# Kernel tuning notes

Measured on AMD Instinct MI355X. Metric: run time of the kernel, lower is better.

The kernel has to match this reference:

```python
import jax, jax.numpy as jnp
import numpy as np

N_FR, N_FV, N_REL, N_VAL, N_KN = 512, 512, 256, 256, 512
TOPK_FR, TOPK_FV, TOPK_REL, TOPK_VAL = 8, 8, 4, 6
EPS = 1e-8


def setup_inputs() -> dict:
    key = jax.random.key(0)
    k1, k2, k3, k4 = jax.random.split(key, 4)
    B, S, D, DS = 8, 2048, 2048, 64
    N = N_FR + N_FV + N_REL + N_VAL + N_KN  # 2304
    return {
        "x": jax.random.normal(k1, (B, S, D), dtype=jnp.float32),
        "importance": jax.random.uniform(k2, (B, S), dtype=jnp.float32),
        "W": jax.random.normal(k3, (DS, D), dtype=jnp.float32) * (1.0 / np.sqrt(D)),
        "b": jnp.zeros((DS,), dtype=jnp.float32),
        "neuron_emb": jax.random.normal(k4, (N, DS), dtype=jnp.float32) * 0.02,
    }


def _topk_sparsify(w, k):
    # w: [B, n] -> keep top-k values, zero the rest, renormalize to sum 1
    vals, idx = jax.lax.top_k(w, k)
    B = w.shape[0]
    sparse = jnp.zeros_like(w).at[jnp.arange(B)[:, None], idx].set(vals)
    return sparse / (sparse.sum(axis=-1, keepdims=True) + EPS)


def reference(x, importance, W, b, neuron_emb):
    # Projection (nn.Linear): [B,S,d_space]; dropout is identity in eval mode
    h = jnp.einsum('bsd,kd->bsk', x, W) + b
    # Normalized neuron embeddings (F.normalize along dim=-1)
    emb = neuron_emb / jnp.linalg.norm(neuron_emb, axis=-1, keepdims=True)
    # All routing logits in one shot: [B, S, total_neurons]
    all_logits = jnp.einsum('bsk,nk->bsn', h, emb)

    fr_end = N_FR
    fv_end = N_FR + N_FV
    rel_end = fv_end + N_REL
    val_end = rel_end + N_VAL

    fr_pref = jax.nn.softmax(all_logits[..., :fr_end], axis=-1)
    fv_pref = jax.nn.softmax(all_logits[..., fr_end:fv_end], axis=-1)
    rel_pref = jax.nn.softmax(all_logits[..., fv_end:rel_end], axis=-1)  # shared by Q and K
    val_pref = jax.nn.softmax(all_logits[..., rel_end:val_end], axis=-1)

    def dense(pref):
        return jnp.einsum('bs,bsn->bn', importance, pref)

    fr_w = _topk_sparsify(dense(fr_pref), TOPK_FR)
    fv_w = _topk_sparsify(dense(fv_pref), TOPK_FV)
    rel_d = dense(rel_pref)
    rq_w = _topk_sparsify(rel_d, TOPK_REL)
    rk_w = rq_w  # relational_Q and relational_K slices are identical
    val_w = _topk_sparsify(dense(val_pref), TOPK_VAL)

    # Concatenate the five per-batch routing weight vectors: [B, 512+512+256+256+256]
    return jnp.concatenate([fr_w, fv_w, rq_w, rk_w, val_w], axis=-1)
```

## Files before the change

kernel.cpp:

```cpp
#include <hip/hip_runtime.h>
#include <hip/hip_bf16.h>
#include <hip/hip_fp16.h>

#define B_    8
#define S_    2048
#define D_    2048
#define DS_   64
#define NUSED 1536
#define TOK   16384

typedef __attribute__((ext_vector_type(8))) short bf16x8;
typedef __attribute__((ext_vector_type(4))) float f32x4;

static constexpr int WS_ETF   = 0;
static constexpr int WS_HT    = 98304;
static constexpr int WS_HF    = 2195456;
static constexpr int WS_PART  = 3244032;
static constexpr int WS_PART2 = 4816896;
static constexpr int WS_WF    = 4915200;

__device__ inline short bf_hi(float f, float& rhi) {
    __hip_bfloat16 h = __float2bfloat16(f);
    rhi = __bfloat162float(h);
    return __builtin_bit_cast(short, h);
}
__device__ inline short bf_of(float f) {
    __hip_bfloat16 h = __float2bfloat16(f);
    return __builtin_bit_cast(short, h);
}
__device__ inline int sliceOfTile(int tile) {
    return tile < 32 ? 0 : tile < 64 ? 1 : tile < 80 ? 2 : 3;
}

__launch_bounds__(256)
__global__ void k_wsplit(const float* __restrict__ W, short* __restrict__ wfrag) {
    const int t = threadIdx.x, kstep = blockIdx.x;
    const int msub = t >> 6, lane = t & 63;
    const int m = msub * 16 + (lane & 15);
    const float* wp = W + m * D_ + kstep * 32 + (lane >> 4) * 8;
    float4 a = *reinterpret_cast<const float4*>(wp);
    float4 b = *reinterpret_cast<const float4*>(wp + 4);
    float f[8] = {a.x, a.y, a.z, a.w, b.x, b.y, b.z, b.w};
    bf16x8 hi, lo;
#pragma unroll
    for (int j = 0; j < 8; ++j) {
        float r;
        hi[j] = bf_hi(f[j], r);
        lo[j] = bf_of(f[j] - r);
    }
    short* dst = wfrag + (((kstep << 2) | msub) * 64 + lane) * 16;
    *reinterpret_cast<bf16x8*>(dst)     = hi;
    *reinterpret_cast<bf16x8*>(dst + 8) = lo;
}

__launch_bounds__(128)
__global__ void k_embpack(const float* __restrict__ emb, short* __restrict__ etfrag) {
    __shared__ float red[16][8];
    __shared__ float rn[16];
    const int tid = threadIdx.x;
    const int kh = tid >> 6, lane = tid & 63;
    const int tile = blockIdx.x;
    const int nl = lane & 15;
    const int n = tile * 16 + nl;
    const int kb = kh * 32 + (lane >> 4) * 8;
    const float* ep = emb + n * DS_ + kb;
    float4 a = *reinterpret_cast<const float4*>(ep);
    float4 b = *reinterpret_cast<const float4*>(ep + 4);
    float f[8] = {a.x, a.y, a.z, a.w, b.x, b.y, b.z, b.w};
    float ss = 0.f;
#pragma unroll
    for (int j = 0; j < 8; ++j) ss += f[j] * f[j];
    red[nl][kh * 4 + (lane >> 4)] = ss;
    __syncthreads();
    if (tid < 16) {
        float s = 0.f;
#pragma unroll
        for (int j = 0; j < 8; ++j) s += red[tid][j];
        rn[tid] = 1.0f / sqrtf(s);
    }
    __syncthreads();
    const float r0 = rn[nl];
    bf16x8 hi, lo;
#pragma unroll
    for (int j = 0; j < 8; ++j) {
        float v = f[j] * r0, r;
        hi[j] = bf_hi(v, r);
        lo[j] = bf_of(v - r);
    }
    short* dst = etfrag + (size_t)((tile * 2 + kh) * 64 + lane) * 16;
    *reinterpret_cast<bf16x8*>(dst)     = hi;
    *reinterpret_cast<bf16x8*>(dst + 8) = lo;
}

#define MFMA16(A, Bv, C) __builtin_amdgcn_mfma_f32_16x16x32_bf16(A, Bv, C, 0, 0, 0)

__launch_bounds__(256, 2)
__global__ void k_gemm1(const float* __restrict__ x, const short* __restrict__ wfrag,
                        float* __restrict__ htp) {
    const int tid   = threadIdx.x;
    const int split = blockIdx.x & 1;
    const int tb    = (blockIdx.x >> 1) * 64;
    const int wave  = tid >> 6, lane = tid & 63;
    const int tok   = tb + wave * 16 + (lane & 15);

    const float* xp = x + (size_t)tok * D_ + split * 1024 + (lane >> 4) * 8;
    const short* wp = wfrag + split * 32 * 4096 + lane * 16;

    f32x4 acc0 = {0.f, 0.f, 0.f, 0.f};
    f32x4 acc1 = acc0, acc2 = acc0, acc3 = acc0;

    float4 xa = *reinterpret_cast<const float4*>(xp);
    float4 xb = *reinterpret_cast<const float4*>(xp + 4);

#pragma unroll 2
    for (int ks = 0; ks < 32; ++ks) {
        const short* wk = wp + ks * 4096;
        bf16x8 ah0 = *reinterpret_cast<const bf16x8*>(wk);
        bf16x8 al0 = *reinterpret_cast<const bf16x8*>(wk + 8);
        bf16x8 ah1 = *reinterpret_cast<const bf16x8*>(wk + 1024);
        bf16x8 al1 = *reinterpret_cast<const bf16x8*>(wk + 1032);
        bf16x8 ah2 = *reinterpret_cast<const bf16x8*>(wk + 2048);
        bf16x8 al2 = *reinterpret_cast<const bf16x8*>(wk + 2056);
        bf16x8 ah3 = *reinterpret_cast<const bf16x8*>(wk + 3072);
        bf16x8 al3 = *reinterpret_cast<const bf16x8*>(wk + 3080);

        float xf[8] = {xa.x, xa.y, xa.z, xa.w, xb.x, xb.y, xb.z, xb.w};
        bf16x8 bh, bl;
#pragma unroll
        for (int j = 0; j < 8; ++j) {
            float r;
            bh[j] = bf_hi(xf[j], r);
            bl[j] = bf_of(xf[j] - r);
        }
        if (ks < 31) {
            xa = *reinterpret_cast<const float4*>(xp + (ks + 1) * 32);
            xb = *reinterpret_cast<const float4*>(xp + (ks + 1) * 32 + 4);
        }
        acc0 = MFMA16(ah0, bh, acc0);
        acc1 = MFMA16(ah1, bh, acc1);
        acc2 = MFMA16(ah2, bh, acc2);
        acc3 = MFMA16(ah3, bh, acc3);
        acc0 = MFMA16(al0, bh, acc0);
        acc1 = MFMA16(al1, bh, acc1);
        acc2 = MFMA16(al2, bh, acc2);
        acc3 = MFMA16(al3, bh, acc3);
        acc0 = MFMA16(ah0, bl, acc0);
        acc1 = MFMA16(ah1, bl, acc1);
        acc2 = MFMA16(ah2, bl, acc2);
        acc3 = MFMA16(ah3, bl, acc3);
    }

    const int row0 = split * 64 + (lane >> 4) * 4;
    const int col  = tb + wave * 16 + (lane & 15);
#pragma unroll
    for (int r = 0; r < 4; ++r) {
        htp[(size_t)(row0 +  0 + r) * TOK + col] = acc0[r];
        htp[(size_t)(row0 + 16 + r) * TOK + col] = acc1[r];
        htp[(size_t)(row0 + 32 + r) * TOK + col] = acc2[r];
        htp[(size_t)(row0 + 48 + r) * TOK + col] = acc3[r];
    }
}

__launch_bounds__(256)
__global__ void k_hfix(const float* __restrict__ htp, const float* __restrict__ bias,
                       short* __restrict__ hfrag) {
    const int idx = blockIdx.x * 256 + threadIdx.x;
    const int tt = idx >> 7, rem = idx & 127;
    const int kh = rem >> 6, lane = rem & 63;
    const int t = tt * 16 + (lane & 15);
    const int kb = kh * 32 + (lane >> 4) * 8;
    bf16x8 hi, lo;
#pragma unroll
    for (int j = 0; j < 8; ++j) {
        const int k = kb + j;
        float v = htp[(size_t)k * TOK + t] + htp[(size_t)(k + 64) * TOK + t] + bias[k];
        float r;
        hi[j] = bf_hi(v, r);
        lo[j] = bf_of(v - r);
    }
    short* dst = hfrag + (size_t)((tt * 2 + kh) * 64 + lane) * 16;
    *reinterpret_cast<bf16x8*>(dst)     = hi;
    *reinterpret_cast<bf16x8*>(dst + 8) = lo;
}

__launch_bounds__(512, 2)
__global__ void k_route2(const short* __restrict__ hfrag, const short* __restrict__ etfrag,
                         const float* __restrict__ imp, float* __restrict__ part) {
    __shared__ float zw[8][2][16];
    __shared__ float coef[4][16];
    __shared__ float impb[16];

    const int tid = threadIdx.x;
    const int w = tid >> 6, lane = tid & 63;
    const int tt = blockIdx.x;
    const int tk = lane & 15, g = lane >> 4;

    const short* hp = hfrag + (size_t)(tt * 2) * 1024 + lane * 16;
    bf16x8 bh0 = *reinterpret_cast<const bf16x8*>(hp);
    bf16x8 bl0 = *reinterpret_cast<const bf16x8*>(hp + 8);
    bf16x8 bh1 = *reinterpret_cast<const bf16x8*>(hp + 1024);
    bf16x8 bl1 = *reinterpret_cast<const bf16x8*>(hp + 1032);

    if (tid < 16) impb[tid] = imp[tt * 16 + tid];

    const int t0 = w * 12;
    const int sA = sliceOfTile(t0);
    const int sB = sliceOfTile(t0 + 11);
    float zacc0 = 0.f, zacc1 = 0.f;
    float p[12][4];

    const short* ep = etfrag + (size_t)t0 * 2048 + lane * 16;
#pragma unroll
    for (int ti = 0; ti < 12; ++ti) {
        const short* cp = ep + (size_t)ti * 2048;
        bf16x8 ah0 = *reinterpret_cast<const bf16x8*>(cp);
        bf16x8 al0 = *reinterpret_cast<const bf16x8*>(cp + 8);
        bf16x8 ah1 = *reinterpret_cast<const bf16x8*>(cp + 1024);
        bf16x8 al1 = *reinterpret_cast<const bf16x8*>(cp + 1032);
        f32x4 a0 = {0.f, 0.f, 0.f, 0.f};
        f32x4 a1 = {0.f, 0.f, 0.f, 0.f};
        a0 = MFMA16(ah0, bh0, a0);
        a1 = MFMA16(ah1, bh1, a1);
        a0 = MFMA16(al0, bh0, a0);
        a1 = MFMA16(al1, bh1, a1);
        a0 = MFMA16(ah0, bl0, a0);
        a1 = MFMA16(ah1, bl1, a1);
        const float p0 = __expf(a0[0] + a1[0]);
        const float p1 = __expf(a0[1] + a1[1]);
        const float p2 = __expf(a0[2] + a1[2]);
        const float p3 = __expf(a0[3] + a1[3]);
        p[ti][0] = p0; p[ti][1] = p1; p[ti][2] = p2; p[ti][3] = p3;
        const float zs = (p0 + p1) + (p2 + p3);
        if (sliceOfTile(t0 + ti) == sA) zacc0 += zs; else zacc1 += zs;
    }

    zacc0 += __shfl_xor(zacc0, 16); zacc0 += __shfl_xor(zacc0, 32);
    zacc1 += __shfl_xor(zacc1, 16); zacc1 += __shfl_xor(zacc1, 32);
    if (lane < 16) { zw[w][0][lane] = zacc0; zw[w][1][lane] = zacc1; }
    __syncthreads();

    if (tid < 64) {
        const int s = tid >> 4, k2 = tid & 15;
        float z = 0.f;
#pragma unroll
        for (int w2 = 0; w2 < 8; ++w2) {
            const int a = sliceOfTile(w2 * 12);
            const int b = sliceOfTile(w2 * 12 + 11);
            if (a == s) z += zw[w2][0][k2];
            if (b == s && b != a) z += zw[w2][1][k2];
        }
        coef[s][k2] = impb[k2] / z;
    }
    __syncthreads();

    const float cA = coef[sA][tk];
    const float cB = coef[sB][tk];
    float* pout = part + (size_t)tt * NUSED;
#pragma unroll
    for (int ti = 0; ti < 12; ++ti) {
        const float c = (sliceOfTile(t0 + ti) == sA) ? cA : cB;
        float v0 = p[ti][0] * c, v1 = p[ti][1] * c, v2 = p[ti][2] * c, v3 = p[ti][3] * c;
#pragma unroll
        for (int st = 1; st < 16; st <<= 1) {
            v0 += __shfl_xor(v0, st);
            v1 += __shfl_xor(v1, st);
            v2 += __shfl_xor(v2, st);
            v3 += __shfl_xor(v3, st);
        }
        if (tk == 0)
            *reinterpret_cast<float4*>(&pout[(t0 + ti) * 16 + g * 4]) =
                make_float4(v0, v1, v2, v3);
    }
}

__launch_bounds__(256)
__global__ void kA(const float* __restrict__ part, float* __restrict__ part2) {
    const int tid = threadIdx.x;
    const int b = blockIdx.x >> 3, g = blockIdx.x & 7;
    const int base = (b * 128 + g * 16) * NUSED;
#pragma unroll
    for (int i = 0; i < 6; ++i) {
        int n = tid + 256 * i;
        float s = 0.f;
#pragma unroll
        for (int r = 0; r < 16; ++r) s += part[base + r * NUSED + n];
        part2[(b * 8 + g) * NUSED + n] = s;
    }
}

__launch_bounds__(256)
__global__ void kB(const float* __restrict__ part2, float* __restrict__ out) {
    __shared__ float dens[NUSED];
    __shared__ float s_v[4][8];
    __shared__ int   s_n[4][8];
    const int tid = threadIdx.x;
    const int b = blockIdx.x;

#pragma unroll
    for (int i = 0; i < 6; ++i) {
        int n = tid + 256 * i;
        float s = 0.f;
#pragma unroll
        for (int g = 0; g < 8; ++g) s += part2[(b * 8 + g) * NUSED + n];
        dens[n] = s;
    }
    for (int i = tid; i < 1792; i += 256) out[b * 1792 + i] = 0.f;
    __syncthreads();

    const int w = tid >> 6, lane = tid & 63;
    const int soffs[4] = {0, 512, 1024, 1280};
    const int ssz[4]   = {512, 512, 256, 256};
    const int kks[4]   = {8, 8, 4, 6};
    const int ooffs[4] = {0, 512, 1024, 1536};
    const int Sn = ssz[w], soff = soffs[w], kk = kks[w];
    const int nslots = Sn >> 6;

    float v[8];
#pragma unroll
    for (int i = 0; i < 8; ++i)
        v[i] = (i < nslots) ? dens[soff + lane + 64 * i] : -1e30f;

    unsigned rm = 0;
    float ssum = 0.f;
    for (int it = 0; it < kk; ++it) {
        float bv = -1e30f;
        int bn = 0x7fffffff;
#pragma unroll
        for (int i = 0; i < 8; ++i) {
            bool valid = (i < nslots) && !((rm >> i) & 1u);
            if (valid && v[i] > bv) { bv = v[i]; bn = lane + 64 * i; }
        }
#pragma unroll
        for (int off = 32; off; off >>= 1) {
            float ov = __shfl_xor(bv, off);
            int   on = __shfl_xor(bn, off);
            if (ov > bv || (ov == bv && on < bn)) { bv = ov; bn = on; }
        }
        ssum += bv;
        if ((bn & 63) == lane) rm |= 1u << (bn >> 6);
        if (lane == 0) { s_v[w][it] = bv; s_n[w][it] = bn; }
    }
    const float inv = 1.f / (ssum + 1e-8f);
    if (lane < kk) {
        int n = s_n[w][lane];
        float val = s_v[w][lane] * inv;
        out[b * 1792 + ooffs[w] + n] = val;
        if (w == 2) out[b * 1792 + 1280 + n] = val;
    }
}

extern "C" void kernel_launch(void* const* d_in, const int* in_sizes, int n_in,
                              void* d_out, int out_size, void* d_ws, size_t ws_size,
                              hipStream_t stream) {
    const float* x    = (const float*)d_in[0];
    const float* imp  = (const float*)d_in[1];
    const float* W    = (const float*)d_in[2];
    const float* bias = (const float*)d_in[3];
    const float* emb  = (const float*)d_in[4];
    float* out = (float*)d_out;
    float* ws  = (float*)d_ws;

    short* etfrag = (short*)(ws + WS_ETF);
    float* htp    = ws + WS_HT;
    short* hfrag  = (short*)(ws + WS_HF);
    float* part   = ws + WS_PART;
    float* part2  = ws + WS_PART2;
    short* wfrag  = (short*)(ws + WS_WF);

    k_embpack<<<96, 128, 0, stream>>>(emb, etfrag);
    k_wsplit<<<64, 256, 0, stream>>>(W, wfrag);
    k_gemm1<<<512, 256, 0, stream>>>(x, wfrag, htp);
    k_hfix<<<512, 256, 0, stream>>>(htp, bias, hfrag);
    k_route2<<<1024, 512, 0, stream>>>(hfrag, etfrag, imp, part);
    kA<<<64, 256, 0, stream>>>(part, part2);
    kB<<<8, 256, 0, stream>>>(part2, out);
}
```

Baseline: 92.13 us.

## Stage W fragments in double-buffered LDS via global_load_lds in gemm1

The W fragment layout is changed so the hi and lo halves sit in separate contiguous 512-element runs. gemm1 now stages each k-step's 8 KB of W fragments into a double-buffered shared-memory tile with direct global-to-LDS loads, instead of having every wave load them from global memory. The aim is to cut redundant global/L2 traffic for W, which all four waves share, and to overlap the next step's load with the MFMAs. The cost is a __syncthreads per k-step plus 16 KB of LDS per block, which could limit occupancy at two blocks per CU. There is also no explicit wait on the async LDS loads (vmcnt) before reading, so correctness relies on the barrier lowering.

```diff
diff --git a/kernel.cpp b/kernel.cpp
--- a/kernel.cpp
+++ b/kernel.cpp
@@ -18,6 +18,9 @@
 static constexpr int WS_PART  = 3244032;
 static constexpr int WS_PART2 = 4816896;
 static constexpr int WS_WF    = 4915200;
+
+typedef __attribute__((address_space(1))) const void g_void;
+typedef __attribute__((address_space(3))) void l_void;
 
 __device__ inline short bf_hi(float f, float& rhi) {
     __hip_bfloat16 h = __float2bfloat16(f);
@@ -48,9 +51,9 @@
         hi[j] = bf_hi(f[j], r);
         lo[j] = bf_of(f[j] - r);
     }
-    short* dst = wfrag + (((kstep << 2) | msub) * 64 + lane) * 16;
-    *reinterpret_cast<bf16x8*>(dst)     = hi;
-    *reinterpret_cast<bf16x8*>(dst + 8) = lo;
+    short* base = wfrag + (size_t)(kstep * 4 + msub) * 1024;
+    *reinterpret_cast<bf16x8*>(base + lane * 8)       = hi;
+    *reinterpret_cast<bf16x8*>(base + 512 + lane * 8) = lo;
 }
 
 __launch_bounds__(128)
@@ -97,32 +100,37 @@
 __launch_bounds__(256, 2)
 __global__ void k_gemm1(const float* __restrict__ x, const short* __restrict__ wfrag,
                         float* __restrict__ htp) {
+    __shared__ short wlds[2][4096];
+
     const int tid   = threadIdx.x;
     const int split = blockIdx.x & 1;
     const int tb    = (blockIdx.x >> 1) * 64;
     const int wave  = tid >> 6, lane = tid & 63;
     const int tok   = tb + wave * 16 + (lane & 15);
 
-    const float* xp = x + (size_t)tok * D_ + split * 1024 + (lane >> 4) * 8;
-    const short* wp = wfrag + split * 32 * 4096 + lane * 16;
+    const float* xp   = x + (size_t)tok * D_ + split * 1024 + (lane >> 4) * 8;
+    const short* wsrc = wfrag + (size_t)(split * 32) * 4096;
 
     f32x4 acc0 = {0.f, 0.f, 0.f, 0.f};
     f32x4 acc1 = acc0, acc2 = acc0, acc3 = acc0;
 
+    __builtin_amdgcn_global_load_lds((g_void*)(wsrc + tid * 8),
+                                     (l_void*)(&wlds[0][tid * 8]), 16, 0, 0);
+    __builtin_amdgcn_global_load_lds((g_void*)(wsrc + 2048 + tid * 8),
+                                     (l_void*)(&wlds[0][2048 + tid * 8]), 16, 0, 0);
     float4 xa = *reinterpret_cast<const float4*>(xp);
     float4 xb = *reinterpret_cast<const float4*>(xp + 4);
 
-#pragma unroll 2
     for (int ks = 0; ks < 32; ++ks) {
-        const short* wk = wp + ks * 4096;
-        bf16x8 ah0 = *reinterpret_cast<const bf16x8*>(wk);
-        bf16x8 al0 = *reinterpret_cast<const bf16x8*>(wk + 8);
-        bf16x8 ah1 = *reinterpret_cast<const bf16x8*>(wk + 1024);
-        bf16x8 al1 = *reinterpret_cast<const bf16x8*>(wk + 1032);
-        bf16x8 ah2 = *reinterpret_cast<const bf16x8*>(wk + 2048);
-        bf16x8 al2 = *reinterpret_cast<const bf16x8*>(wk + 2056);
-        bf16x8 ah3 = *reinterpret_cast<const bf16x8*>(wk + 3072);
-        bf16x8 al3 = *reinterpret_cast<const bf16x8*>(wk + 3080);
+        __syncthreads();
+        const int buf = ks & 1;
+        if (ks < 31) {
+            const short* ns = wsrc + (size_t)(ks + 1) * 4096;
+            __builtin_amdgcn_global_load_lds((g_void*)(ns + tid * 8),
+                                             (l_void*)(&wlds[buf ^ 1][tid * 8]), 16, 0, 0);
+            __builtin_amdgcn_global_load_lds((g_void*)(ns + 2048 + tid * 8),
+                                             (l_void*)(&wlds[buf ^ 1][2048 + tid * 8]), 16, 0, 0);
+        }
 
         float xf[8] = {xa.x, xa.y, xa.z, xa.w, xb.x, xb.y, xb.z, xb.w};
         bf16x8 bh, bl;
@@ -136,6 +144,17 @@
             xa = *reinterpret_cast<const float4*>(xp + (ks + 1) * 32);
             xb = *reinterpret_cast<const float4*>(xp + (ks + 1) * 32 + 4);
         }
+
+        const short* wl = &wlds[buf][0];
+        bf16x8 ah0 = *reinterpret_cast<const bf16x8*>(wl +    0 + lane * 8);
+        bf16x8 al0 = *reinterpret_cast<const bf16x8*>(wl +  512 + lane * 8);
+        bf16x8 ah1 = *reinterpret_cast<const bf16x8*>(wl + 1024 + lane * 8);
+        bf16x8 al1 = *reinterpret_cast<const bf16x8*>(wl + 1536 + lane * 8);
+        bf16x8 ah2 = *reinterpret_cast<const bf16x8*>(wl + 2048 + lane * 8);
+        bf16x8 al2 = *reinterpret_cast<const bf16x8*>(wl + 2560 + lane * 8);
+        bf16x8 ah3 = *reinterpret_cast<const bf16x8*>(wl + 3072 + lane * 8);
+        bf16x8 al3 = *reinterpret_cast<const bf16x8*>(wl + 3584 + lane * 8);
+
         acc0 = MFMA16(ah0, bh, acc0);
         acc1 = MFMA16(ah1, bh, acc1);
         acc2 = MFMA16(ah2, bh, acc2);
```

Result: faster. 87.42 us (-5.1%).
